# Kernel tuning notes

Measured on AMD Instinct MI355X. Metric: run time of the kernel, lower is better.

## Reference

```python
import jax, jax.numpy as jnp
import numpy as np

PIXEL_W = 1.0
EPS = 1e-8
BIG = 1e10


def extract_zero_crossings(s):
    """Vectorized marching-squares-style zero-crossing extraction.
    s: (H, W) SDF. Returns padded points (N, 2) float and validity mask (N,) bool,
    N = (H-1)*W + H*(W-1), in the same (vertical pairs first, then horizontal)
    order as the original python loops."""
    H, W = s.shape
    dt = s.dtype
    # vertical neighbor pairs (i, j) vs (i+1, j)
    v1, v2 = s[:-1, :], s[1:, :]
    ii = jnp.broadcast_to(jnp.arange(H - 1, dtype=dt)[:, None], (H - 1, W))
    jj = jnp.broadcast_to(jnp.arange(W, dtype=dt)[None, :], (H - 1, W))
    c1 = v1 == 0
    c2 = (~c1) & (v2 == 0)
    cx = (~c1) & (~c2) & (v1 * v2 < 0)
    alpha = jnp.abs(v1) / (jnp.abs(v1) + jnp.abs(v2) + EPS)
    row = jnp.where(c1, ii, jnp.where(c2, ii + 1.0, ii + alpha))
    pts_v = jnp.stack([row, jj], axis=-1).reshape(-1, 2)
    m_v = (c1 | c2 | cx).reshape(-1)
    # horizontal neighbor pairs (i, j) vs (i, j+1)
    h1, h2 = s[:, :-1], s[:, 1:]
    ii2 = jnp.broadcast_to(jnp.arange(H, dtype=dt)[:, None], (H, W - 1))
    jj2 = jnp.broadcast_to(jnp.arange(W - 1, dtype=dt)[None, :], (H, W - 1))
    d1 = h1 == 0
    d2 = (~d1) & (h2 == 0)
    dx = (~d1) & (~d2) & (h1 * h2 < 0)
    beta = jnp.abs(h1) / (jnp.abs(h1) + jnp.abs(h2) + EPS)
    col = jnp.where(d1, jj2, jnp.where(d2, jj2 + 1.0, jj2 + beta))
    pts_h = jnp.stack([ii2, col], axis=-1).reshape(-1, 2)
    m_h = (d1 | d2 | dx).reshape(-1)
    return jnp.concatenate([pts_v, pts_h], 0), jnp.concatenate([m_v, m_h], 0)


def pairwise_dist(p, g):
    # (Np, Ng) euclidean distances via the gram trick (avoids (Np,Ng,2) temp)
    d2 = jnp.sum(p * p, 1)[:, None] + jnp.sum(g * g, 1)[None, :] - 2.0 * (p @ g.T)
    return jnp.sqrt(jnp.maximum(d2, 0.0))


def masked_chamfer(pp, pm, gp, gm):
    # chamfer as in compute_chamfer_distance: -mean(min over gt) + mean(min over pred)
    d = pairwise_dist(pp, gp)
    d = jnp.where(pm[:, None] & gm[None, :], d, BIG)
    min_p = jnp.min(d, axis=1)
    min_g = jnp.min(d, axis=0)
    np_ = jnp.maximum(jnp.sum(pm), 1)
    ng_ = jnp.maximum(jnp.sum(gm), 1)
    return -jnp.sum(jnp.where(pm, min_p, 0.0)) / np_ + jnp.sum(jnp.where(gm, min_g, 0.0)) / ng_


def setup_inputs() -> dict:
    key = jax.random.key(0)
    k1, k2 = jax.random.split(key)
    B, H, W = 2, 80, 80
    return {
        "pred_logits": jax.random.normal(k1, (B, 1, H, W), dtype=jnp.float32),
        "gt_sdf": jax.random.normal(k2, (B, 1, H, W), dtype=jnp.float32),
    }


def reference(pred_logits, gt_sdf):
    pred = pred_logits[:, 0]  # (B, H, W)
    gt = gt_sdf[:, 0]
    pixel_loss = jnp.mean(jnp.abs(pred - gt))
    chamfers = []
    for b in range(pred.shape[0]):  # small fixed batch loop
        pp, pm = extract_zero_crossings(pred[b])
        gp, gm = extract_zero_crossings(gt[b])
        chamfers.append(masked_chamfer(pp, pm, gp, gm))
    loss = PIXEL_W * pixel_loss
    last_chamfer = jnp.mean(jnp.stack(chamfers))
    return loss, last_chamfer
```

## Files before the change

kernel.cpp:

```cpp
#include <hip/hip_runtime.h>

#define HH 80
#define WW 80
#define IMG (HH * WW)
#define NV ((HH - 1) * WW)
#define NPTS (NV + HH * (WW - 1))
#define NPIX (2 * IMG)
#define BIGF 1.0e10f
#define INVC 1.0e7f
#define EPSF 1e-8f
#define QSCALE 131072.0f

#define SETPAD 12800
#define SBLOCKS (SETPAD / 256)
#define EXBLOCKS (4 * SBLOCKS)
#define PXBLOCKS (NPIX / 256)
#define PREPB (EXBLOCKS + PXBLOCKS)

#define BLK 256
#define APT 8
#define ACHUNK (BLK * APT)
#define ABLOCKS ((NPTS + ACHUNK - 1) / ACHUNK)
#define NSLICE 32
#define MAXSLICE ((((NPTS + NSLICE - 1) / NSLICE) + 1) & ~1)
#define MAXP2 (MAXSLICE / 2)

#define CNT_STRIDE 32
#define PIX_OFF 512
#define TICKET_OFF 640
#define SUM_OFF 768
#define SCALAR_BYTES 1024

typedef float f32x2 __attribute__((ext_vector_type(2)));

__device__ __forceinline__ long long wave_reduce_ll(long long v) {
#pragma unroll
  for (int o = 32; o > 0; o >>= 1) {
    int2 p = *(int2*)&v;
    p.x = __shfl_down(p.x, o, 64);
    p.y = __shfl_down(p.y, o, 64);
    v += *(long long*)&p;
  }
  return v;
}

__global__ void k_zero(unsigned int* __restrict__ w) {
  w[threadIdx.x] = 0u;
}

__global__ void __launch_bounds__(256) k_prep(
    const float* __restrict__ pred, const float* __restrict__ gt,
    float2* __restrict__ pts, float* __restrict__ minarr,
    int* __restrict__ cnt, unsigned long long* __restrict__ pix_i) {
  __shared__ int wc[4], wo[4];
  __shared__ long long rl[4];
  int tid = threadIdx.x, lane = tid & 63, wid = tid >> 6;
  int gtid = blockIdx.x * 256 + tid;

  if (gtid < 4 * NPTS) minarr[gtid] = BIGF;

  if (blockIdx.x < EXBLOCKS) {
    int set = blockIdx.x / SBLOCKS;
    int idx = (blockIdx.x % SBLOCKS) * 256 + tid;
    const float* s = (set < 2 ? pred : gt) + (set & 1) * IMG;
    float r = 0.f, c = 0.f;
    bool valid = false;
    if (idx < NPTS) {
      if (idx < NV) {
        int i = idx / WW, j = idx - i * WW;
        float v1 = s[i * WW + j], v2 = s[(i + 1) * WW + j];
        c = (float)j;
        if (v1 == 0.f)      { r = (float)i;       valid = true; }
        else if (v2 == 0.f) { r = (float)i + 1.f; valid = true; }
        else {
          r = (float)i + fabsf(v1) / (fabsf(v1) + fabsf(v2) + EPSF);
          valid = (v1 * v2 < 0.f);
        }
      } else {
        int t = idx - NV;
        int i = t / (WW - 1), j = t - i * (WW - 1);
        float h1 = s[i * WW + j], h2 = s[i * WW + j + 1];
        r = (float)i;
        if (h1 == 0.f)      { c = (float)j;       valid = true; }
        else if (h2 == 0.f) { c = (float)j + 1.f; valid = true; }
        else {
          c = (float)j + fabsf(h1) / (fabsf(h1) + fabsf(h2) + EPSF);
          valid = (h1 * h2 < 0.f);
        }
      }
    }
    unsigned long long mask = __ballot(valid);
    int nw = __popcll(mask);
    if (lane == 0) wc[wid] = nw;
    __syncthreads();
    if (tid == 0) {
      int t0 = wc[0], t1 = wc[1], t2 = wc[2], t3 = wc[3];
      int tot = t0 + t1 + t2 + t3;
      int base = tot ? atomicAdd(&cnt[set * CNT_STRIDE], tot) : 0;
      wo[0] = base; wo[1] = base + t0; wo[2] = base + t0 + t1;
      wo[3] = base + t0 + t1 + t2;
    }
    __syncthreads();
    if (valid) {
      int lpos = __popcll(mask & ((1ull << lane) - 1ull));
      pts[set * NPTS + wo[wid] + lpos] = make_float2(r, c);
    }
  } else {
    int p = (blockIdx.x - EXBLOCKS) * 256 + tid;
    float d = fabsf(pred[p] - gt[p]);
    long long q = (long long)(d * QSCALE + 0.5f);
    q = wave_reduce_ll(q);
    if (lane == 0) rl[wid] = q;
    __syncthreads();
    if (tid == 0)
      atomicAdd(pix_i, (unsigned long long)(rl[0] + rl[1] + rl[2] + rl[3]));
  }
}

__global__ void __launch_bounds__(BLK) k_min(
    const float2* __restrict__ pts, float* __restrict__ minarr,
    const int* __restrict__ cnt) {
  int dir = blockIdx.z;
  int Aset = ((dir & 1) << 1) | (dir >> 1);
  int Bset = Aset ^ 2;
  int cntA = cnt[Aset * CNT_STRIDE], cntB = cnt[Bset * CNT_STRIDE];

  int abase0 = blockIdx.x * ACHUNK;
  if (abase0 >= cntA) return;
  int slicelen = (((cntB + NSLICE - 1) / NSLICE) + 1) & ~1;
  int b0 = blockIdx.y * slicelen;
  if (b0 >= cntB) return;
  int n = min(slicelen, cntB - b0);
  int sn = (n + 1) & ~1;

  __shared__ f32x2 qx_s[MAXP2], qy_s[MAXP2], q2_s[MAXP2];
  for (int i = threadIdx.x; i < sn; i += BLK) {
    float2 q = (i < n) ? pts[Bset * NPTS + b0 + i] : make_float2(INVC, INVC);
    ((float*)qx_s)[i] = q.x;
    ((float*)qy_s)[i] = q.y;
    ((float*)q2_s)[i] = fmaf(q.x, q.x, q.y * q.y);
  }
  __syncthreads();

  int abase = abase0 + threadIdx.x;
  f32x2 nxv[APT], nyv[APT];
  float p2v[APT], m[APT];
#pragma unroll
  for (int i = 0; i < APT; ++i) {
    int a = abase + i * BLK;
    float2 p = (a < cntA) ? pts[Aset * NPTS + a] : make_float2(0.f, 0.f);
    float nx = -2.f * p.x, ny = -2.f * p.y;
    nxv[i].x = nx; nxv[i].y = nx;
    nyv[i].x = ny; nyv[i].y = ny;
    p2v[i] = fmaf(p.x, p.x, p.y * p.y);
    m[i] = 3.0e38f;
  }

  int np2 = sn >> 1;
#pragma unroll 2
  for (int p = 0; p < np2; ++p) {
    f32x2 qx = qx_s[p], qy = qy_s[p], q2 = q2_s[p];
#pragma unroll
    for (int i = 0; i < APT; ++i) {
      f32x2 u = __builtin_elementwise_fma(
          nyv[i], qy, __builtin_elementwise_fma(nxv[i], qx, q2));
      m[i] = fminf(fminf(u.x, u.y), m[i]);
    }
  }

#pragma unroll
  for (int i = 0; i < APT; ++i) {
    int a = abase + i * BLK;
    if (a < cntA) {
      float d2 = fmaxf(m[i] + p2v[i], 0.f);
      atomicMin((unsigned int*)&minarr[Aset * NPTS + a], __float_as_uint(d2));
    }
  }
}

__global__ void __launch_bounds__(256) k_fin(
    const float* __restrict__ minarr, const int* __restrict__ cnt,
    const unsigned long long* __restrict__ pix_i,
    unsigned long long* __restrict__ sum_i,
    unsigned int* __restrict__ ticket, float* __restrict__ out) {
  int set = blockIdx.x >> 2, q = blockIdx.x & 3;
  int tid = threadIdx.x, lane = tid & 63;
  int n = cnt[set * CNT_STRIDE];

  long long ls = 0;
  for (int i = q * 256 + tid; i < n; i += 1024) {
    float d = sqrtf(minarr[set * NPTS + i]);
    ls += (long long)(d * QSCALE + 0.5f);
  }
  ls = wave_reduce_ll(ls);
  if (lane == 0) atomicAdd(&sum_i[set], (unsigned long long)ls);
  __syncthreads();

  if (tid == 0) {
    __threadfence();
    unsigned int t = atomicAdd(ticket, 1u);
    if (t == 15u) {
      const float iq = 1.0f / QSCALE;
      float ss[4];
      for (int k = 0; k < 4; ++k)
        ss[k] = (float)((long long)atomicAdd(&sum_i[k], 0ull)) * iq;
      float n0 = fmaxf((float)cnt[0 * CNT_STRIDE], 1.f);
      float n1 = fmaxf((float)cnt[1 * CNT_STRIDE], 1.f);
      float n2 = fmaxf((float)cnt[2 * CNT_STRIDE], 1.f);
      float n3 = fmaxf((float)cnt[3 * CNT_STRIDE], 1.f);
      float ch0 = -ss[0] / n0 + ss[2] / n2;
      float ch1 = -ss[1] / n1 + ss[3] / n3;
      out[0] = (float)(long long)(*pix_i) * iq / (float)NPIX;
      out[1] = 0.5f * (ch0 + ch1);
    }
  }
}

extern "C" void kernel_launch(void* const* d_in, const int* in_sizes, int n_in,
                              void* d_out, int out_size, void* d_ws, size_t ws_size,
                              hipStream_t stream) {
  const float* pred = (const float*)d_in[0];
  const float* gt   = (const float*)d_in[1];
  float* out = (float*)d_out;

  int* cnt = (int*)d_ws;
  unsigned long long* pix_i = (unsigned long long*)((char*)d_ws + PIX_OFF);
  unsigned int* ticket = (unsigned int*)((char*)d_ws + TICKET_OFF);
  unsigned long long* sum_i = (unsigned long long*)((char*)d_ws + SUM_OFF);
  float2* pts   = (float2*)((char*)d_ws + SCALAR_BYTES);
  float* minarr = (float*)((char*)d_ws + SCALAR_BYTES + sizeof(float2) * 4 * NPTS);

  k_zero<<<1, 256, 0, stream>>>((unsigned int*)d_ws);
  k_prep<<<PREPB, 256, 0, stream>>>(pred, gt, pts, minarr, cnt, pix_i);
  k_min<<<dim3(ABLOCKS, NSLICE, 4), BLK, 0, stream>>>(pts, minarr, cnt);
  k_fin<<<16, 256, 0, stream>>>(minarr, cnt, pix_i, sum_i, ticket, out);
}
```

Measured before the change: 38.47 us.

## Replace atomicMin scatter with per-slice partial minima reduced in finalize kernel

k_min now writes each slice's per-point minimum into a dedicated partial row instead of issuing atomicMin into a shared min array, and k_fin reduces the slices before the sqrt/sum. This removes the BIG initialization in k_prep and the atomic contention across the 32 slices. The cost is a larger workspace buffer and a finalize kernel that now reads up to 32 rows per point, using only 16 blocks. MAXAI=13 assumes at most about 3328 points per set chunk, which holds for count up to 13312.

```diff
diff --git a/kernel.cpp b/kernel.cpp
--- a/kernel.cpp
+++ b/kernel.cpp
@@ -24,6 +24,11 @@
 #define NSLICE 32
 #define MAXSLICE ((((NPTS + NSLICE - 1) / NSLICE) + 1) & ~1)
 #define MAXP2 (MAXSLICE / 2)
+#define AROW 6400
+
+#define MAXAI 7
+#undef MAXAI
+#define MAXAI 13
 
 #define CNT_STRIDE 32
 #define PIX_OFF 512
@@ -50,14 +55,11 @@
 
 __global__ void __launch_bounds__(256) k_prep(
     const float* __restrict__ pred, const float* __restrict__ gt,
-    float2* __restrict__ pts, float* __restrict__ minarr,
-    int* __restrict__ cnt, unsigned long long* __restrict__ pix_i) {
+    float2* __restrict__ pts, int* __restrict__ cnt,
+    unsigned long long* __restrict__ pix_i) {
   __shared__ int wc[4], wo[4];
   __shared__ long long rl[4];
   int tid = threadIdx.x, lane = tid & 63, wid = tid >> 6;
-  int gtid = blockIdx.x * 256 + tid;
-
-  if (gtid < 4 * NPTS) minarr[gtid] = BIGF;
 
   if (blockIdx.x < EXBLOCKS) {
     int set = blockIdx.x / SBLOCKS;
@@ -118,7 +120,7 @@
 }
 
 __global__ void __launch_bounds__(BLK) k_min(
-    const float2* __restrict__ pts, float* __restrict__ minarr,
+    const float2* __restrict__ pts, float* __restrict__ part,
     const int* __restrict__ cnt) {
   int dir = blockIdx.z;
   int Aset = ((dir & 1) << 1) | (dir >> 1);
@@ -168,29 +170,48 @@
     }
   }
 
+  float* row = part + (size_t)(dir * NSLICE + blockIdx.y) * AROW;
 #pragma unroll
   for (int i = 0; i < APT; ++i) {
     int a = abase + i * BLK;
-    if (a < cntA) {
-      float d2 = fmaxf(m[i] + p2v[i], 0.f);
-      atomicMin((unsigned int*)&minarr[Aset * NPTS + a], __float_as_uint(d2));
-    }
+    if (a < cntA) row[a] = fmaxf(m[i] + p2v[i], 0.f);
   }
 }
 
 __global__ void __launch_bounds__(256) k_fin(
-    const float* __restrict__ minarr, const int* __restrict__ cnt,
+    const float* __restrict__ part, const int* __restrict__ cnt,
     const unsigned long long* __restrict__ pix_i,
     unsigned long long* __restrict__ sum_i,
     unsigned int* __restrict__ ticket, float* __restrict__ out) {
-  int set = blockIdx.x >> 2, q = blockIdx.x & 3;
+  int set = blockIdx.x >> 2, chunk = blockIdx.x & 3;
   int tid = threadIdx.x, lane = tid & 63;
+  int dir = ((set & 1) << 1) | (set >> 1);
   int n = cnt[set * CNT_STRIDE];
-
+  int cntB = cnt[(set ^ 2) * CNT_STRIDE];
+  int slicelen = (((cntB + NSLICE - 1) / NSLICE) + 1) & ~1;
+  int nsv = (slicelen > 0) ? min(NSLICE, (cntB + slicelen - 1) / slicelen) : 0;
+  const float* base = part + (size_t)dir * NSLICE * AROW;
+
+  int c0 = (n + 3) >> 2;
+  int a0 = chunk * c0;
+  int a1 = min(a0 + c0, n);
+
+  float mm[MAXAI];
+#pragma unroll
+  for (int i = 0; i < MAXAI; ++i) mm[i] = BIGF;
+  for (int s = 0; s < nsv; ++s) {
+    const float* r = base + (size_t)s * AROW;
+#pragma unroll
+    for (int i = 0; i < MAXAI; ++i) {
+      int a = a0 + i * 256 + tid;
+      if (a < a1) mm[i] = fminf(mm[i], r[a]);
+    }
+  }
   long long ls = 0;
-  for (int i = q * 256 + tid; i < n; i += 1024) {
-    float d = sqrtf(minarr[set * NPTS + i]);
-    ls += (long long)(d * QSCALE + 0.5f);
+#pragma unroll
+  for (int i = 0; i < MAXAI; ++i) {
+    int a = a0 + i * 256 + tid;
+    if (a < a1) ls += (long long)(sqrtf(mm[i]) * QSCALE + 0.5f);
   }
   ls = wave_reduce_ll(ls);
   if (lane == 0) atomicAdd(&sum_i[set], (unsigned long long)ls);
@@ -227,11 +248,11 @@
   unsigned long long* pix_i = (unsigned long long*)((char*)d_ws + PIX_OFF);
   unsigned int* ticket = (unsigned int*)((char*)d_ws + TICKET_OFF);
   unsigned long long* sum_i = (unsigned long long*)((char*)d_ws + SUM_OFF);
-  float2* pts   = (float2*)((char*)d_ws + SCALAR_BYTES);
-  float* minarr = (float*)((char*)d_ws + SCALAR_BYTES + sizeof(float2) * 4 * NPTS);
+  float2* pts = (float2*)((char*)d_ws + SCALAR_BYTES);
+  float* part = (float*)((char*)d_ws + SCALAR_BYTES + sizeof(float2) * 4 * NPTS);
 
   k_zero<<<1, 256, 0, stream>>>((unsigned int*)d_ws);
-  k_prep<<<PREPB, 256, 0, stream>>>(pred, gt, pts, minarr, cnt, pix_i);
-  k_min<<<dim3(ABLOCKS, NSLICE, 4), BLK, 0, stream>>>(pts, minarr, cnt);
-  k_fin<<<16, 256, 0, stream>>>(minarr, cnt, pix_i, sum_i, ticket, out);
-}
+  k_prep<<<PREPB, 256, 0, stream>>>(pred, gt, pts, cnt, pix_i);
+  k_min<<<dim3(ABLOCKS, NSLICE, 4), BLK, 0, stream>>>(pts, part, cnt);
+  k_fin<<<16, 256, 0, stream>>>(part, cnt, pix_i, sum_i, ticket, out);
+}
```

New measurement: 93.03 us. 2.42x slower.
